# Kernel optimization log

Measured on AMD Instinct MI355X. Metric: run time of the kernel, lower is better.

## Reference

```python
import jax, jax.numpy as jnp
import numpy as np

B, N, DIM, H, DH, M = 2, 2048, 1024, 16, 64, 512
INNER = H * DH  # 1024
KV = M + 1 + N  # xl mem + null kv + sequence = 2561


def rotate_half(x):
    x1, x2 = jnp.split(x, 2, axis=-1)
    return jnp.concatenate([-x2, x1], axis=-1)


def apply_rotary_pos_emb(pos, t):
    return t * jnp.cos(pos) + rotate_half(t) * jnp.sin(pos)


def setup_inputs() -> dict:
    key = jax.random.key(0)
    ks = jax.random.split(key, 8)
    return {
        "x": jax.random.normal(ks[0], (B, N, DIM), jnp.float32),
        "rotary_q": jax.random.uniform(ks[1], (N, DH), jnp.float32) * 6.28,
        "rotary_k": jax.random.uniform(ks[2], (KV, DH), jnp.float32) * 6.28,
        "xl_memories": jax.random.normal(ks[3], (2, B, H, M, DH), jnp.float32) * 0.02,
        "Wq": jax.random.normal(ks[4], (DIM, INNER), jnp.float32) * 0.02,
        "Wkv": jax.random.normal(ks[5], (DIM, 2 * INNER), jnp.float32) * 0.02,
        "Wout": jax.random.normal(ks[6], (INNER, INNER), jnp.float32) * 0.02,
        "null_kv": jax.random.normal(ks[7], (2, H, DH), jnp.float32),
    }


def reference(x, rotary_q, rotary_k, xl_memories, Wq, Wkv, Wout, null_kv):
    # QKV projections (no bias, matching keras Dense(use_bias=False))
    q = (x @ Wq).reshape(B, N, H, DH).transpose(0, 2, 1, 3)  # b h n d
    k, v = jnp.split(x @ Wkv, 2, axis=-1)
    k = k.reshape(B, N, H, DH).transpose(0, 2, 1, 3)
    v = v.reshape(B, N, H, DH).transpose(0, 2, 1, 3)

    # prepend learned null key/value (1 token)
    nk = jnp.broadcast_to(null_kv[0][None, :, None, :], (B, H, 1, DH))
    nv = jnp.broadcast_to(null_kv[1][None, :, None, :], (B, H, 1, DH))
    k = jnp.concatenate([nk, k], axis=2)
    v = jnp.concatenate([nv, v], axis=2)

    next_xl_memories = jnp.stack([k, v])  # [2, b, h, 1+n, d]

    # prepend XL memories along key axis
    k = jnp.concatenate([xl_memories[0], k], axis=2)  # b h kv d
    v = jnp.concatenate([xl_memories[1], v], axis=2)

    # inline rotary embedding on q and (full) k
    q = apply_rotary_pos_emb(rotary_q, q)
    k = apply_rotary_pos_emb(rotary_k, k)

    # causal attention with bottom-right aligned mask (mem/null tokens visible)
    scale = DH ** -0.5
    sim = jnp.einsum('bhid,bhjd->bhij', q, k) * scale  # b h n kv
    i = jnp.arange(N)[:, None]
    j = jnp.arange(KV)[None, :]
    causal_ok = j <= (i + (KV - N))
    sim = jnp.where(causal_ok, sim, jnp.finfo(sim.dtype).min)
    attn = jax.nn.softmax(sim, axis=-1)
    out = jnp.einsum('bhij,bhjd->bhid', attn, v)  # b h n d

    out = out.transpose(0, 2, 1, 3).reshape(B, N, INNER)
    return out @ Wout, next_xl_memories
```

## Files before the change

kernel.cpp:

```cpp
#include <hip/hip_runtime.h>
#include <hip/hip_bf16.h>


typedef short v8s __attribute__((ext_vector_type(8)));
typedef float v4f __attribute__((ext_vector_type(4)));

__device__ __forceinline__ float bf2f(unsigned short x) {
  return __uint_as_float(((unsigned)x) << 16);
}
__device__ __forceinline__ unsigned short f2bf(float f) {
  unsigned u = __float_as_uint(f);
  u += 0x7FFFu + ((u >> 16) & 1u);
  return (unsigned short)(u >> 16);
}

#if __has_builtin(__builtin_amdgcn_exp2f)
#define EXP2(x) __builtin_amdgcn_exp2f(x)
#else
#define EXP2(x) exp2f(x)
#endif

__device__ __forceinline__ void gld_lds16(const void* g, void* l) {
  __builtin_amdgcn_global_load_lds(
      (const __attribute__((address_space(1))) unsigned int*)g,
      (__attribute__((address_space(3))) unsigned int*)l, 16, 0, 0);
}

__device__ __forceinline__ unsigned pk_bf16(float lo, float hi) {
  union { __hip_bfloat162 h; unsigned u; } cv;
  cv.h = __float22bfloat162_rn(make_float2(lo, hi));
  return cv.u;
}

__global__ __launch_bounds__(256) void cvt_bf16(
    const float* __restrict__ S, unsigned short* __restrict__ D, int n4)
{
  const int i = blockIdx.x * 256 + threadIdx.x;
  if (i < n4) {
    const float4 v = ((const float4*)S)[i];
    ushort4 o;
    o.x = f2bf(v.x); o.y = f2bf(v.y); o.z = f2bf(v.z); o.w = f2bf(v.w);
    ((ushort4*)D)[i] = o;
  }
}

template <typename CT>
__global__ __launch_bounds__(256, 2) void gemm_bf16(
    const unsigned short* __restrict__ A,
    const unsigned short* __restrict__ WT,
    CT* __restrict__ C,
    int K, int ldc)
{
  __shared__ unsigned short As[128 * 64];
  __shared__ unsigned short Bs[128 * 64];
  const int tid  = threadIdx.x;
  const int wave = tid >> 6, lane = tid & 63;
  const int l15  = lane & 15, quad = lane >> 4;
  const int wm   = wave >> 1, wn = wave & 1;
  const int row0 = blockIdx.x * 128, col0 = blockIdx.y * 128;
  const int lrow = lane >> 3;
  const int gsw  = (lane & 7) ^ lrow;

  v4f acc[4][4];
  const v4f vzero = {0.f, 0.f, 0.f, 0.f};
#pragma unroll
  for (int i = 0; i < 4; ++i)
#pragma unroll
    for (int j = 0; j < 4; ++j) acc[i][j] = vzero;

  for (int k0 = 0; k0 < K; k0 += 64) {
    __syncthreads();
#pragma unroll
    for (int ro = 0; ro < 4; ++ro) {
      const int chunk = wave * 4 + ro;
      const int arow  = chunk * 8 + lrow;
      gld_lds16(A  + (size_t)(row0 + arow) * K + k0 + gsw * 8, As + chunk * 512);
      gld_lds16(WT + (size_t)(col0 + arow) * K + k0 + gsw * 8, Bs + chunk * 512);
    }
    __syncthreads();

    v8s af[4][2], bf[4][2];
#pragma unroll
    for (int tm = 0; tm < 4; ++tm) {
      const int r = wm * 64 + tm * 16 + l15;
#pragma unroll
      for (int kk = 0; kk < 2; ++kk) {
        const int slot = (kk * 4 + quad) ^ (r & 7);
        af[tm][kk] = *(const v8s*)(As + r * 64 + slot * 8);
      }
    }
#pragma unroll
    for (int tn = 0; tn < 4; ++tn) {
      const int r = wn * 64 + tn * 16 + l15;
#pragma unroll
      for (int kk = 0; kk < 2; ++kk) {
        const int slot = (kk * 4 + quad) ^ (r & 7);
        bf[tn][kk] = *(const v8s*)(Bs + r * 64 + slot * 8);
      }
    }
#pragma unroll
    for (int kk = 0; kk < 2; ++kk)
#pragma unroll
      for (int tm = 0; tm < 4; ++tm)
#pragma unroll
        for (int tn = 0; tn < 4; ++tn)
          acc[tm][tn] = __builtin_amdgcn_mfma_f32_16x16x32_bf16(
              af[tm][kk], bf[tn][kk], acc[tm][tn], 0, 0, 0);
  }

#pragma unroll
  for (int tm = 0; tm < 4; ++tm)
#pragma unroll
    for (int tn = 0; tn < 4; ++tn)
#pragma unroll
      for (int r = 0; r < 4; ++r) {
        const int row = row0 + wm * 64 + tm * 16 + quad * 4 + r;
        const int col = col0 + wn * 64 + tn * 16 + l15;
        if constexpr (sizeof(CT) == 2)
          C[(size_t)row * ldc + col] = (CT)f2bf(acc[tm][tn][r]);
        else
          C[(size_t)row * ldc + col] = (CT)acc[tm][tn][r];
      }
}

__global__ __launch_bounds__(256) void transpose_wt(
    const float* __restrict__ S0,
    const float* __restrict__ S1,
    int c0, int c1, int K,
    unsigned short* __restrict__ D)
{
  __shared__ float T[64][65];
  const int k0 = blockIdx.x * 64, n0 = blockIdx.y * 64;
  const int tid = threadIdx.x;
#pragma unroll
  for (int ro = 0; ro < 4; ++ro) {
    const int idx = ro * 256 + tid;
    const int kr = idx >> 4, ch = idx & 15;
    const int n = n0 + ch * 4;
    float4 val;
    if (n < c0) val = *(const float4*)(S0 + (size_t)(k0 + kr) * c0 + n);
    else        val = *(const float4*)(S1 + (size_t)(k0 + kr) * c1 + (n - c0));
    T[kr][ch * 4 + 0] = val.x; T[kr][ch * 4 + 1] = val.y;
    T[kr][ch * 4 + 2] = val.z; T[kr][ch * 4 + 3] = val.w;
  }
  __syncthreads();
#pragma unroll
  for (int ro = 0; ro < 2; ++ro) {
    const int idx = ro * 256 + tid;
    const int nl = idx >> 3, ch = idx & 7;
    __align__(16) unsigned short tmp[8];
#pragma unroll
    for (int e = 0; e < 8; ++e) tmp[e] = f2bf(T[ch * 8 + e][nl]);
    *(uint4*)(D + (size_t)(n0 + nl) * K + k0 + ch * 8) = *(const uint4*)tmp;
  }
}

__global__ __launch_bounds__(256) void assemble(
    const unsigned short* __restrict__ QKV,
    const float* __restrict__ rq,
    const float* __restrict__ rk,
    const float* __restrict__ xlm,
    const float* __restrict__ nkv,
    unsigned short* __restrict__ Qrot,
    unsigned short* __restrict__ Kf,
    unsigned short* __restrict__ Vn,
    float* __restrict__ nxl)
{
  const int gw = blockIdx.x * 4 + (threadIdx.x >> 6);
  const int d  = threadIdx.x & 63;
  const int RK = 32 * 2561;
  const int RQ = 32 * 2048;
  if (gw < RK) {
    const int bh = gw / 2561;
    const int j  = gw - bh * 2561;
    const int b  = bh >> 4, h = bh & 15;
    float kx, vx;
    if (j < 512) {
      const size_t i0 = (((size_t)(b * 16 + h)) * 512 + j) * 64 + d;
      kx = xlm[i0];
      vx = xlm[1048576 + i0];
    } else if (j == 512) {
      kx = nkv[h * 64 + d];
      vx = nkv[1024 + h * 64 + d];
    } else {
      const size_t rowb = ((size_t)(b * 2048 + (j - 513))) * 3072;
      kx = bf2f(QKV[rowb + 1024 + h * 64 + d]);
      vx = bf2f(QKV[rowb + 2048 + h * 64 + d]);
    }
    Vn[(((size_t)bh) * 2561 + j) * 64 + d] = f2bf(vx);
    if (j >= 512) {
      const size_t o0 = (((size_t)(b * 16 + h)) * 2049 + (j - 512)) * 64 + d;
      nxl[o0] = kx;
      nxl[4196352 + o0] = vx;
    }
    const float ang = rk[j * 64 + d];
    const float cs = __cosf(ang), sn = __sinf(ang);
    const float part = __shfl_xor(kx, 32);
    const float kr = kx * cs + (d < 32 ? -part : part) * sn;
    Kf[(((size_t)bh) * 2624 + j) * 64 + d] = f2bf(kr);
  } else if (gw < RK + RQ) {
    const int g2 = gw - RK;
    const int bh = g2 >> 11, n = g2 & 2047;
    const int b  = bh >> 4, h = bh & 15;
    const float qx = bf2f(QKV[((size_t)(b * 2048 + n)) * 3072 + h * 64 + d]);
    const float ang = rq[n * 64 + d];
    const float cs = __cosf(ang), sn = __sinf(ang);
    const float part = __shfl_xor(qx, 32);
    const float qr = qx * cs + (d < 32 ? -part : part) * sn;
    Qrot[(((size_t)bh) * 2048 + n) * 64 + d] = f2bf(qr * 0.18033688f);
  } else {
    const int g3 = gw - RK - RQ;
    const int bh = g3 / 63;
    const int jj = 2561 + (g3 - bh * 63);
    Kf[(((size_t)bh) * 2624 + jj) * 64 + d] = 0;
  }
}

__global__ __launch_bounds__(256) void transpose_v(
    const unsigned short* __restrict__ Vn,
    unsigned short* __restrict__ VTp)
{
  __shared__ unsigned short T[64][72];
  const int j0 = blockIdx.x * 64;
  const int bh = blockIdx.y;
  const int tid = threadIdx.x;
#pragma unroll
  for (int ro = 0; ro < 2; ++ro) {
    const int idx = ro * 256 + tid;
    const int jr = idx >> 3, ch = idx & 7;
    uint4 val = make_uint4(0, 0, 0, 0);
    if (j0 + jr < 2561)
      val = *(const uint4*)(Vn + (((size_t)bh) * 2561 + j0 + jr) * 64 + ch * 8);
    *(uint4*)(&T[jr][ch * 8]) = val;
  }
  __syncthreads();
#pragma unroll
  for (int ro = 0; ro < 2; ++ro) {
    const int idx = ro * 256 + tid;
    const int dl = idx >> 3, ch = idx & 7;
    __align__(16) unsigned short tmp[8];
#pragma unroll
    for (int e = 0; e < 8; ++e) {
      const int kappa = ch * 8 + e;
      const int sig = (kappa & 32) + ((e & 4) << 2) + ((ch & 3) << 2) + (e & 3);
      tmp[e] = T[sig][dl];
    }
    *(uint4*)(VTp + (((size_t)bh) * 64 + dl) * 2624 + j0 + ch * 8) = *(const uint4*)tmp;
  }
}

__global__ __launch_bounds__(128, 2) void attn_fa(
    const unsigned short* __restrict__ Qr,
    const unsigned short* __restrict__ Kf,
    const unsigned short* __restrict__ VTp,
    unsigned short* __restrict__ Ao)
{
  const int bh = blockIdx.y;
  const int qb = 31 - (int)((blockIdx.x + blockIdx.y) & 31);
  const int b = bh >> 4, h = bh & 15;
  __shared__ unsigned short Ks[2][64 * 72];
  __shared__ unsigned short Vs[2][64 * 72];
  const int tid = threadIdx.x;
  const int wave = tid >> 6;
  const int lane = tid & 63;
  const int l15 = lane & 15, quad = lane >> 4;
  const v4f vzero = {0.f, 0.f, 0.f, 0.f};

  v8s qf00, qf01, qf10, qf11;
  {
    const unsigned short* Qg0 =
        Qr + (((size_t)bh) * 2048 + qb * 64 + wave * 32 + l15) * 64;
    qf00 = *(const v8s*)(Qg0 + quad * 8);
    qf01 = *(const v8s*)(Qg0 + 32 + quad * 8);
    const unsigned short* Qg1 = Qg0 + 16 * 64;
    qf10 = *(const v8s*)(Qg1 + quad * 8);
    qf11 = *(const v8s*)(Qg1 + 32 + quad * 8);
  }
  const int qb0 = qb * 64 + wave * 32 + l15 + 513;

  v4f O00 = vzero, O01 = vzero, O02 = vzero, O03 = vzero;
  v4f O10 = vzero, O11 = vzero, O12 = vzero, O13 = vzero;
  v4f Ol0 = vzero, Ol1 = vzero;
  const short one_bf = (short)0x3F80;
  const v8s ones = {one_bf, one_bf, one_bf, one_bf,
                    one_bf, one_bf, one_bf, one_bf};

  const unsigned short* Kg0 = Kf + (size_t)bh * 2624 * 64;
  const unsigned short* Vg0 = VTp + (size_t)bh * 64 * 2624;
  const int ntiles = (qb + 10 <= 41) ? (qb + 10) : 41;
  const int tfast  = qb + 7;

  const int srow = tid >> 3, sch = tid & 7;
  uint4 kk0, kk1, kk2, kk3, vv0, vv1, vv2, vv3;

#define PREFETCH(t)                                                          \
  {                                                                          \
    const int j0p = (t) * 64;                                                \
    kk0 = *(const uint4*)(Kg0 + (size_t)(j0p + srow)      * 64 + sch * 8);   \
    kk1 = *(const uint4*)(Kg0 + (size_t)(j0p + srow + 16) * 64 + sch * 8);   \
    kk2 = *(const uint4*)(Kg0 + (size_t)(j0p + srow + 32) * 64 + sch * 8);   \
    kk3 = *(const uint4*)(Kg0 + (size_t)(j0p + srow + 48) * 64 + sch * 8);   \
    vv0 = *(const uint4*)(Vg0 + (size_t)(srow)      * 2624 + j0p + sch * 8); \
    vv1 = *(const uint4*)(Vg0 + (size_t)(srow + 16) * 2624 + j0p + sch * 8); \
    vv2 = *(const uint4*)(Vg0 + (size_t)(srow + 32) * 2624 + j0p + sch * 8); \
    vv3 = *(const uint4*)(Vg0 + (size_t)(srow + 48) * 2624 + j0p + sch * 8); \
  }
#define STAGE(bi)                                                            \
  {                                                                          \
    *(uint4*)(Ks[bi] + (srow)      * 72 + sch * 8) = kk0;                    \
    *(uint4*)(Ks[bi] + (srow + 16) * 72 + sch * 8) = kk1;                    \
    *(uint4*)(Ks[bi] + (srow + 32) * 72 + sch * 8) = kk2;                    \
    *(uint4*)(Ks[bi] + (srow + 48) * 72 + sch * 8) = kk3;                    \
    *(uint4*)(Vs[bi] + (srow)      * 72 + sch * 8) = vv0;                    \
    *(uint4*)(Vs[bi] + (srow + 16) * 72 + sch * 8) = vv1;                    \
    *(uint4*)(Vs[bi] + (srow + 32) * 72 + sch * 8) = vv2;                    \
    *(uint4*)(Vs[bi] + (srow + 48) * 72 + sch * 8) = vv3;                    \
  }

  auto compute_tile = [&](const unsigned short* Ksb, const unsigned short* Vsb,
                          int j0, bool masked) {
    v4f s[2][4];
#pragma unroll
    for (int jt = 0; jt < 4; ++jt) {
      const v8s kfr0 = *(const v8s*)(Ksb + (jt * 16 + l15) * 72 + quad * 8);
      const v8s kfr1 = *(const v8s*)(Ksb + (jt * 16 + l15) * 72 + 32 + quad * 8);
      v4f c0 = vzero;
      c0 = __builtin_amdgcn_mfma_f32_16x16x32_bf16(kfr0, qf00, c0, 0, 0, 0);
      c0 = __builtin_amdgcn_mfma_f32_16x16x32_bf16(kfr1, qf01, c0, 0, 0, 0);
      s[0][jt] = c0;
      v4f c1 = vzero;
      c1 = __builtin_amdgcn_mfma_f32_16x16x32_bf16(kfr0, qf10, c1, 0, 0, 0);
      c1 = __builtin_amdgcn_mfma_f32_16x16x32_bf16(kfr1, qf11, c1, 0, 0, 0);
      s[1][jt] = c1;
    }

    if (masked) {
#pragma unroll
      for (int mt = 0; mt < 2; ++mt) {
        const int qbase = qb0 + mt * 16;
#pragma unroll
        for (int jt = 0; jt < 4; ++jt) {
          const int jrow = j0 + jt * 16 + quad * 4;
#pragma unroll
          for (int r = 0; r < 4; ++r)
            s[mt][jt][r] = (jrow + r <= qbase) ? s[mt][jt][r] : -1e30f;
        }
      }
    }

    union PK { unsigned u[4]; v8s s8; };
    PK p0a, p0b, p1a, p1b;
    p0a.u[0] = pk_bf16(EXP2(s[0][0][0]), EXP2(s[0][0][1]));
    p0a.u[1] = pk_bf16(EXP2(s[0][0][2]), EXP2(s[0][0][3]));
    p0a.u[2] = pk_bf16(EXP2(s[0][1][0]), EXP2(s[0][1][1]));
    p0a.u[3] = pk_bf16(EXP2(s[0][1][2]), EXP2(s[0][1][3]));
    p0b.u[0] = pk_bf16(EXP2(s[0][2][0]), EXP2(s[0][2][1]));
    p0b.u[1] = pk_bf16(EXP2(s[0][2][2]), EXP2(s[0][2][3]));
    p0b.u[2] = pk_bf16(EXP2(s[0][3][0]), EXP2(s[0][3][1]));
    p0b.u[3] = pk_bf16(EXP2(s[0][3][2]), EXP2(s[0][3][3]));
    p1a.u[0] = pk_bf16(EXP2(s[1][0][0]), EXP2(s[1][0][1]));
    p1a.u[1] = pk_bf16(EXP2(s[1][0][2]), EXP2(s[1][0][3]));
    p1a.u[2] = pk_bf16(EXP2(s[1][1][0]), EXP2(s[1][1][1]));
    p1a.u[3] = pk_bf16(EXP2(s[1][1][2]), EXP2(s[1][1][3]));
    p1b.u[0] = pk_bf16(EXP2(s[1][2][0]), EXP2(s[1][2][1]));
    p1b.u[1] = pk_bf16(EXP2(s[1][2][2]), EXP2(s[1][2][3]));
    p1b.u[2] = pk_bf16(EXP2(s[1][3][0]), EXP2(s[1][3][1]));
    p1b.u[3] = pk_bf16(EXP2(s[1][3][2]), EXP2(s[1][3][3]));

#pragma unroll
    for (int dt = 0; dt < 4; ++dt) {
      const v8s vf0 = *(const v8s*)(Vsb + (dt * 16 + l15) * 72 + quad * 8);
      const v8s vf1 = *(const v8s*)(Vsb + (dt * 16 + l15) * 72 + 32 + quad * 8);
      v4f c0 = (dt == 0) ? O00 : (dt == 1) ? O01 : (dt == 2) ? O02 : O03;
      c0 = __builtin_amdgcn_mfma_f32_16x16x32_bf16(p0a.s8, vf0, c0, 0, 0, 0);
      c0 = __builtin_amdgcn_mfma_f32_16x16x32_bf16(p0b.s8, vf1, c0, 0, 0, 0);
      if (dt == 0) O00 = c0; else if (dt == 1) O01 = c0;
      else if (dt == 2) O02 = c0; else O03 = c0;
      v4f c1 = (dt == 0) ? O10 : (dt == 1) ? O11 : (dt == 2) ? O12 : O13;
      c1 = __builtin_amdgcn_mfma_f32_16x16x32_bf16(p1a.s8, vf0, c1, 0, 0, 0);
      c1 = __builtin_amdgcn_mfma_f32_16x16x32_bf16(p1b.s8, vf1, c1, 0, 0, 0);
      if (dt == 0) O10 = c1; else if (dt == 1) O11 = c1;
      else if (dt == 2) O12 = c1; else O13 = c1;
    }
    Ol0 = __builtin_amdgcn_mfma_f32_16x16x32_bf16(p0a.s8, ones, Ol0, 0, 0, 0);
    Ol0 = __builtin_amdgcn_mfma_f32_16x16x32_bf16(p0b.s8, ones, Ol0, 0, 0, 0);
    Ol1 = __builtin_amdgcn_mfma_f32_16x16x32_bf16(p1a.s8, ones, Ol1, 0, 0, 0);
    Ol1 = __builtin_amdgcn_mfma_f32_16x16x32_bf16(p1b.s8, ones, Ol1, 0, 0, 0);
  };

  PREFETCH(0);
  STAGE(0);
  PREFETCH(1);
  __syncthreads();
  for (int t = 0; t < ntiles; ++t) {
    if (t + 1 < ntiles) {
      STAGE((t + 1) & 1);
      if (t + 2 < ntiles) PREFETCH(t + 2);
    }
    compute_tile(Ks[t & 1], Vs[t & 1], t * 64, t > tfast);
    __syncthreads();
  }
#undef PREFETCH
#undef STAGE

#pragma unroll
  for (int r = 0; r < 4; ++r) {
    const float linv0 = 1.0f / Ol0[r];
    const int n0 = qb * 64 + wave * 32 + quad * 4 + r;
    const size_t rb0 = ((size_t)b * 2048 + n0) * 1024 + h * 64;
    Ao[rb0 + 0 * 16 + l15] = f2bf(O00[r] * linv0);
    Ao[rb0 + 1 * 16 + l15] = f2bf(O01[r] * linv0);
    Ao[rb0 + 2 * 16 + l15] = f2bf(O02[r] * linv0);
    Ao[rb0 + 3 * 16 + l15] = f2bf(O03[r] * linv0);
    const float linv1 = 1.0f / Ol1[r];
    const size_t rb1 = rb0 + (size_t)16 * 1024;
    Ao[rb1 + 0 * 16 + l15] = f2bf(O10[r] * linv1);
    Ao[rb1 + 1 * 16 + l15] = f2bf(O11[r] * linv1);
    Ao[rb1 + 2 * 16 + l15] = f2bf(O12[r] * linv1);
    Ao[rb1 + 3 * 16 + l15] = f2bf(O13[r] * linv1);
  }
}

extern "C" void kernel_launch(void* const* d_in, const int* in_sizes, int n_in,
                              void* d_out, int out_size, void* d_ws, size_t ws_size,
                              hipStream_t stream)
{
  const float* x    = (const float*)d_in[0];
  const float* rq   = (const float*)d_in[1];
  const float* rk   = (const float*)d_in[2];
  const float* xlm  = (const float*)d_in[3];
  const float* Wq   = (const float*)d_in[4];
  const float* Wkv  = (const float*)d_in[5];
  const float* Wout = (const float*)d_in[6];
  const float* nkv  = (const float*)d_in[7];
  float* out = (float*)d_out;
  float* nxl = out + 4194304;
  char* ws = (char*)d_ws;
  unsigned short* QKV   = (unsigned short*)(ws + 0);
  unsigned short* xbf   = (unsigned short*)(ws + 25165824);
  unsigned short* Ao    = (unsigned short*)(ws + 25165824);
  unsigned short* WqkvT = (unsigned short*)(ws + 33554432);
  unsigned short* WoutT = (unsigned short*)(ws + 39845888);
  unsigned short* Qrot  = (unsigned short*)(ws + 41943040);
  unsigned short* Kf    = (unsigned short*)(ws + 50331648);
  unsigned short* Vn    = (unsigned short*)(ws + 61079552);
  unsigned short* VTp   = (unsigned short*)(ws + 71569408);

  cvt_bf16<<<4096, 256, 0, stream>>>(x, xbf, 1048576);
  transpose_wt<<<dim3(16, 48), 256, 0, stream>>>(Wq, Wkv, 1024, 2048, 1024, WqkvT);
  transpose_wt<<<dim3(16, 16), 256, 0, stream>>>(Wout, Wout, 1024, 1024, 1024, WoutT);
  gemm_bf16<unsigned short><<<dim3(32, 24), 256, 0, stream>>>(xbf, WqkvT, QKV, 1024, 3072);
  assemble<<<37376, 256, 0, stream>>>(QKV, rq, rk, xlm, nkv, Qrot, Kf, Vn, nxl);
  transpose_v<<<dim3(41, 32), 256, 0, stream>>>(Vn, VTp);
  attn_fa<<<dim3(32, 32), 128, 0, stream>>>(Qrot, Kf, VTp, Ao);
  gemm_bf16<float><<<dim3(32, 8), 256, 0, stream>>>(Ao, WoutT, out, 1024, 1024);
}
```

Before: 241.8 us.

## Split KV range across two wave pairs in attention with LDS reduction

The attention block grows from 2 to 4 waves. Two wave pairs each process half of the KV tiles using 32-wide KV tiles, and their partial O and row-sum accumulators are combined through shared memory at the end. This doubles parallelism per query block to hide latency on the long causal KV loop. In exchange it adds a final LDS reduction and an extra barrier, uses smaller tiles with more loop iterations, and puts more register and occupancy pressure on the kernel under launch_bounds(256,4).

```diff
diff --git a/kernel.cpp b/kernel.cpp
--- a/kernel.cpp
+++ b/kernel.cpp
@@ -249,7 +249,7 @@
   }
 }
 
-__global__ __launch_bounds__(128, 2) void attn_fa(
+__global__ __launch_bounds__(256, 4) void attn_fa(
     const unsigned short* __restrict__ Qr,
     const unsigned short* __restrict__ Kf,
     const unsigned short* __restrict__ VTp,
@@ -258,10 +258,12 @@
   const int bh = blockIdx.y;
   const int qb = 31 - (int)((blockIdx.x + blockIdx.y) & 31);
   const int b = bh >> 4, h = bh & 15;
-  __shared__ unsigned short Ks[2][64 * 72];
-  __shared__ unsigned short Vs[2][64 * 72];
+  __shared__ unsigned short Ks[2][2][32 * 72];
+  __shared__ unsigned short Vs[2][2][64 * 40];
   const int tid = threadIdx.x;
   const int wave = tid >> 6;
+  const int wr  = wave & 1;
+  const int kvh = wave >> 1;
   const int lane = tid & 63;
   const int l15 = lane & 15, quad = lane >> 4;
   const v4f vzero = {0.f, 0.f, 0.f, 0.f};
@@ -269,14 +271,14 @@
   v8s qf00, qf01, qf10, qf11;
   {
     const unsigned short* Qg0 =
-        Qr + (((size_t)bh) * 2048 + qb * 64 + wave * 32 + l15) * 64;
+        Qr + (((size_t)bh) * 2048 + qb * 64 + wr * 32 + l15) * 64;
     qf00 = *(const v8s*)(Qg0 + quad * 8);
     qf01 = *(const v8s*)(Qg0 + 32 + quad * 8);
     const unsigned short* Qg1 = Qg0 + 16 * 64;
     qf10 = *(const v8s*)(Qg1 + quad * 8);
     qf11 = *(const v8s*)(Qg1 + 32 + quad * 8);
   }
-  const int qb0 = qb * 64 + wave * 32 + l15 + 513;
+  const int qb0 = qb * 64 + wr * 32 + l15 + 513;
 
   v4f O00 = vzero, O01 = vzero, O02 = vzero, O03 = vzero;
   v4f O10 = vzero, O11 = vzero, O12 = vzero, O13 = vzero;
@@ -287,137 +289,148 @@
 
   const unsigned short* Kg0 = Kf + (size_t)bh * 2624 * 64;
   const unsigned short* Vg0 = VTp + (size_t)bh * 64 * 2624;
-  const int ntiles = (qb + 10 <= 41) ? (qb + 10) : 41;
-  const int tfast  = qb + 7;
-
-  const int srow = tid >> 3, sch = tid & 7;
-  uint4 kk0, kk1, kk2, kk3, vv0, vv1, vv2, vv3;
+  const int nt32  = (2 * qb + 19 <= 81) ? (2 * qb + 19) : 81;
+  const int nh    = (nt32 + 1) >> 1;
+  const int tbase = kvh ? nh : 0;
+  const int tcnt  = kvh ? (nt32 - nh) : nh;
+  const int tfast = 2 * qb + wr + 15;
+
+  const int ptid = tid & 127;
+  const int krow = ptid >> 3, ksch = ptid & 7;
+  const int vrow = ptid >> 2, vscv = ptid & 3;
+  uint4 kk0, kk1, vv0, vv1;
 
 #define PREFETCH(t)                                                          \
   {                                                                          \
-    const int j0p = (t) * 64;                                                \
-    kk0 = *(const uint4*)(Kg0 + (size_t)(j0p + srow)      * 64 + sch * 8);   \
-    kk1 = *(const uint4*)(Kg0 + (size_t)(j0p + srow + 16) * 64 + sch * 8);   \
-    kk2 = *(const uint4*)(Kg0 + (size_t)(j0p + srow + 32) * 64 + sch * 8);   \
-    kk3 = *(const uint4*)(Kg0 + (size_t)(j0p + srow + 48) * 64 + sch * 8);   \
-    vv0 = *(const uint4*)(Vg0 + (size_t)(srow)      * 2624 + j0p + sch * 8); \
-    vv1 = *(const uint4*)(Vg0 + (size_t)(srow + 16) * 2624 + j0p + sch * 8); \
-    vv2 = *(const uint4*)(Vg0 + (size_t)(srow + 32) * 2624 + j0p + sch * 8); \
-    vv3 = *(const uint4*)(Vg0 + (size_t)(srow + 48) * 2624 + j0p + sch * 8); \
+    const int j0p = (t) * 32;                                                \
+    kk0 = *(const uint4*)(Kg0 + (size_t)(j0p + krow)      * 64 + ksch * 8);  \
+    kk1 = *(const uint4*)(Kg0 + (size_t)(j0p + krow + 16) * 64 + ksch * 8);  \
+    vv0 = *(const uint4*)(Vg0 + (size_t)(vrow)      * 2624 + j0p + vscv * 8);\
+    vv1 = *(const uint4*)(Vg0 + (size_t)(vrow + 32) * 2624 + j0p + vscv * 8);\
   }
 #define STAGE(bi)                                                            \
   {                                                                          \
-    *(uint4*)(Ks[bi] + (srow)      * 72 + sch * 8) = kk0;                    \
-    *(uint4*)(Ks[bi] + (srow + 16) * 72 + sch * 8) = kk1;                    \
-    *(uint4*)(Ks[bi] + (srow + 32) * 72 + sch * 8) = kk2;                    \
-    *(uint4*)(Ks[bi] + (srow + 48) * 72 + sch * 8) = kk3;                    \
-    *(uint4*)(Vs[bi] + (srow)      * 72 + sch * 8) = vv0;                    \
-    *(uint4*)(Vs[bi] + (srow + 16) * 72 + sch * 8) = vv1;                    \
-    *(uint4*)(Vs[bi] + (srow + 32) * 72 + sch * 8) = vv2;                    \
-    *(uint4*)(Vs[bi] + (srow + 48) * 72 + sch * 8) = vv3;                    \
+    *(uint4*)(Ks[kvh][bi] + (krow)      * 72 + ksch * 8) = kk0;              \
+    *(uint4*)(Ks[kvh][bi] + (krow + 16) * 72 + ksch * 8) = kk1;              \
+    *(uint4*)(Vs[kvh][bi] + (vrow)      * 40 + vscv * 8) = vv0;              \
+    *(uint4*)(Vs[kvh][bi] + (vrow + 32) * 40 + vscv * 8) = vv1;              \
   }
 
   auto compute_tile = [&](const unsigned short* Ksb, const unsigned short* Vsb,
-                          int j0, bool masked) {
-    v4f s[2][4];
-#pragma unroll
-    for (int jt = 0; jt < 4; ++jt) {
-      const v8s kfr0 = *(const v8s*)(Ksb + (jt * 16 + l15) * 72 + quad * 8);
-      const v8s kfr1 = *(const v8s*)(Ksb + (jt * 16 + l15) * 72 + 32 + quad * 8);
-      v4f c0 = vzero;
-      c0 = __builtin_amdgcn_mfma_f32_16x16x32_bf16(kfr0, qf00, c0, 0, 0, 0);
-      c0 = __builtin_amdgcn_mfma_f32_16x16x32_bf16(kfr1, qf01, c0, 0, 0, 0);
-      s[0][jt] = c0;
-      v4f c1 = vzero;
-      c1 = __builtin_amdgcn_mfma_f32_16x16x32_bf16(kfr0, qf10, c1, 0, 0, 0);
-      c1 = __builtin_amdgcn_mfma_f32_16x16x32_bf16(kfr1, qf11, c1, 0, 0, 0);
-      s[1][jt] = c1;
-    }
-
-    if (masked) {
-#pragma unroll
-      for (int mt = 0; mt < 2; ++mt) {
-        const int qbase = qb0 + mt * 16;
-#pragma unroll
-        for (int jt = 0; jt < 4; ++jt) {
-          const int jrow = j0 + jt * 16 + quad * 4;
-#pragma unroll
-          for (int r = 0; r < 4; ++r)
-            s[mt][jt][r] = (jrow + r <= qbase) ? s[mt][jt][r] : -1e30f;
-        }
+                          int t) {
+    v4f s00, s01, s10, s11;
+    {
+      const v8s ka0 = *(const v8s*)(Ksb + l15 * 72 + quad * 8);
+      const v8s ka1 = *(const v8s*)(Ksb + l15 * 72 + 32 + quad * 8);
+      v4f c = vzero;
+      c = __builtin_amdgcn_mfma_f32_16x16x32_bf16(ka0, qf00, c, 0, 0, 0);
+      c = __builtin_amdgcn_mfma_f32_16x16x32_bf16(ka1, qf01, c, 0, 0, 0);
+      s00 = c;
+      c = vzero;
+      c = __builtin_amdgcn_mfma_f32_16x16x32_bf16(ka0, qf10, c, 0, 0, 0);
+      c = __builtin_amdgcn_mfma_f32_16x16x32_bf16(ka1, qf11, c, 0, 0, 0);
+      s10 = c;
+      const v8s kb0 = *(const v8s*)(Ksb + (16 + l15) * 72 + quad * 8);
+      const v8s kb1 = *(const v8s*)(Ksb + (16 + l15) * 72 + 32 + quad * 8);
+      c = vzero;
+      c = __builtin_amdgcn_mfma_f32_16x16x32_bf16(kb0, qf00, c, 0, 0, 0);
+      c = __builtin_amdgcn_mfma_f32_16x16x32_bf16(kb1, qf01, c, 0, 0, 0);
+      s01 = c;
+      c = vzero;
+      c = __builtin_amdgcn_mfma_f32_16x16x32_bf16(kb0, qf10, c, 0, 0, 0);
+      c = __builtin_amdgcn_mfma_f32_16x16x32_bf16(kb1, qf11, c, 0, 0, 0);
+      s11 = c;
+    }
+
+    if (t > tfast) {
+      const int j0 = t * 32 + quad * 4;
+#pragma unroll
+      for (int r = 0; r < 4; ++r) {
+        s00[r] = (j0 + r      <= qb0)      ? s00[r] : -1e30f;
+        s01[r] = (j0 + 16 + r <= qb0)      ? s01[r] : -1e30f;
+        s10[r] = (j0 + r      <= qb0 + 16) ? s10[r] : -1e30f;
+        s11[r] = (j0 + 16 + r <= qb0 + 16) ? s11[r] : -1e30f;
       }
     }
 
     union PK { unsigned u[4]; v8s s8; };
-    PK p0a, p0b, p1a, p1b;
-    p0a.u[0] = pk_bf16(EXP2(s[0][0][0]), EXP2(s[0][0][1]));
-    p0a.u[1] = pk_bf16(EXP2(s[0][0][2]), EXP2(s[0][0][3]));
-    p0a.u[2] = pk_bf16(EXP2(s[0][1][0]), EXP2(s[0][1][1]));
-    p0a.u[3] = pk_bf16(EXP2(s[0][1][2]), EXP2(s[0][1][3]));
-    p0b.u[0] = pk_bf16(EXP2(s[0][2][0]), EXP2(s[0][2][1]));
-    p0b.u[1] = pk_bf16(EXP2(s[0][2][2]), EXP2(s[0][2][3]));
-    p0b.u[2] = pk_bf16(EXP2(s[0][3][0]), EXP2(s[0][3][1]));
-    p0b.u[3] = pk_bf16(EXP2(s[0][3][2]), EXP2(s[0][3][3]));
-    p1a.u[0] = pk_bf16(EXP2(s[1][0][0]), EXP2(s[1][0][1]));
-    p1a.u[1] = pk_bf16(EXP2(s[1][0][2]), EXP2(s[1][0][3]));
-    p1a.u[2] = pk_bf16(EXP2(s[1][1][0]), EXP2(s[1][1][1]));
-    p1a.u[3] = pk_bf16(EXP2(s[1][1][2]), EXP2(s[1][1][3]));
-    p1b.u[0] = pk_bf16(EXP2(s[1][2][0]), EXP2(s[1][2][1]));
-    p1b.u[1] = pk_bf16(EXP2(s[1][2][2]), EXP2(s[1][2][3]));
-    p1b.u[2] = pk_bf16(EXP2(s[1][3][0]), EXP2(s[1][3][1]));
-    p1b.u[3] = pk_bf16(EXP2(s[1][3][2]), EXP2(s[1][3][3]));
-
-#pragma unroll
-    for (int dt = 0; dt < 4; ++dt) {
-      const v8s vf0 = *(const v8s*)(Vsb + (dt * 16 + l15) * 72 + quad * 8);
-      const v8s vf1 = *(const v8s*)(Vsb + (dt * 16 + l15) * 72 + 32 + quad * 8);
-      v4f c0 = (dt == 0) ? O00 : (dt == 1) ? O01 : (dt == 2) ? O02 : O03;
-      c0 = __builtin_amdgcn_mfma_f32_16x16x32_bf16(p0a.s8, vf0, c0, 0, 0, 0);
-      c0 = __builtin_amdgcn_mfma_f32_16x16x32_bf16(p0b.s8, vf1, c0, 0, 0, 0);
-      if (dt == 0) O00 = c0; else if (dt == 1) O01 = c0;
-      else if (dt == 2) O02 = c0; else O03 = c0;
-      v4f c1 = (dt == 0) ? O10 : (dt == 1) ? O11 : (dt == 2) ? O12 : O13;
-      c1 = __builtin_amdgcn_mfma_f32_16x16x32_bf16(p1a.s8, vf0, c1, 0, 0, 0);
-      c1 = __builtin_amdgcn_mfma_f32_16x16x32_bf16(p1b.s8, vf1, c1, 0, 0, 0);
-      if (dt == 0) O10 = c1; else if (dt == 1) O11 = c1;
-      else if (dt == 2) O12 = c1; else O13 = c1;
-    }
-    Ol0 = __builtin_amdgcn_mfma_f32_16x16x32_bf16(p0a.s8, ones, Ol0, 0, 0, 0);
-    Ol0 = __builtin_amdgcn_mfma_f32_16x16x32_bf16(p0b.s8, ones, Ol0, 0, 0, 0);
-    Ol1 = __builtin_amdgcn_mfma_f32_16x16x32_bf16(p1a.s8, ones, Ol1, 0, 0, 0);
-    Ol1 = __builtin_amdgcn_mfma_f32_16x16x32_bf16(p1b.s8, ones, Ol1, 0, 0, 0);
+    PK p0, p1;
+    p0.u[0] = pk_bf16(EXP2(s00[0]), EXP2(s00[1]));
+    p0.u[1] = pk_bf16(EXP2(s00[2]), EXP2(s00[3]));
+    p0.u[2] = pk_bf16(EXP2(s01[0]), EXP2(s01[1]));
+    p0.u[3] = pk_bf16(EXP2(s01[2]), EXP2(s01[3]));
+    p1.u[0] = pk_bf16(EXP2(s10[0]), EXP2(s10[1]));
+    p1.u[1] = pk_bf16(EXP2(s10[2]), EXP2(s10[3]));
+    p1.u[2] = pk_bf16(EXP2(s11[0]), EXP2(s11[1]));
+    p1.u[3] = pk_bf16(EXP2(s11[2]), EXP2(s11[3]));
+
+    {
+      const v8s vf0 = *(const v8s*)(Vsb + l15 * 40 + quad * 8);
+      O00 = __builtin_amdgcn_mfma_f32_16x16x32_bf16(p0.s8, vf0, O00, 0, 0, 0);
+      O10 = __builtin_amdgcn_mfma_f32_16x16x32_bf16(p1.s8, vf0, O10, 0, 0, 0);
+      const v8s vf1 = *(const v8s*)(Vsb + (16 + l15) * 40 + quad * 8);
+      O01 = __builtin_amdgcn_mfma_f32_16x16x32_bf16(p0.s8, vf1, O01, 0, 0, 0);
+      O11 = __builtin_amdgcn_mfma_f32_16x16x32_bf16(p1.s8, vf1, O11, 0, 0, 0);
+      const v8s vf2 = *(const v8s*)(Vsb + (32 + l15) * 40 + quad * 8);
+      O02 = __builtin_amdgcn_mfma_f32_16x16x32_bf16(p0.s8, vf2, O02, 0, 0, 0);
+      O12 = __builtin_amdgcn_mfma_f32_16x16x32_bf16(p1.s8, vf2, O12, 0, 0, 0);
+      const v8s vf3 = *(const v8s*)(Vsb + (48 + l15) * 40 + quad * 8);
+      O03 = __builtin_amdgcn_mfma_f32_16x16x32_bf16(p0.s8, vf3, O03, 0, 0, 0);
+      O13 = __builtin_amdgcn_mfma_f32_16x16x32_bf16(p1.s8, vf3, O13, 0, 0, 0);
+    }
+    Ol0 = __builtin_amdgcn_mfma_f32_16x16x32_bf16(p0.s8, ones, Ol0, 0, 0, 0);
+    Ol1 = __builtin_amdgcn_mfma_f32_16x16x32_bf16(p1.s8, ones, Ol1, 0, 0, 0);
   };
 
-  PREFETCH(0);
+  PREFETCH(tbase);
   STAGE(0);
-  PREFETCH(1);
+  PREFETCH(tbase + 1);
   __syncthreads();
-  for (int t = 0; t < ntiles; ++t) {
-    if (t + 1 < ntiles) {
-      STAGE((t + 1) & 1);
-      if (t + 2 < ntiles) PREFETCH(t + 2);
-    }
-    compute_tile(Ks[t & 1], Vs[t & 1], t * 64, t > tfast);
+  for (int it = 0; it < nh; ++it) {
+    if (it < tcnt) {
+      if (it + 1 < tcnt) {
+        STAGE((it + 1) & 1);
+        if (it + 2 < tcnt) PREFETCH(tbase + it + 2);
+      }
+      compute_tile(Ks[kvh][it & 1], Vs[kvh][it & 1], tbase + it);
+    }
     __syncthreads();
   }
 #undef PREFETCH
 #undef STAGE
 
-#pragma unroll
-  for (int r = 0; r < 4; ++r) {
-    const float linv0 = 1.0f / Ol0[r];
-    const int n0 = qb * 64 + wave * 32 + quad * 4 + r;
-    const size_t rb0 = ((size_t)b * 2048 + n0) * 1024 + h * 64;
-    Ao[rb0 + 0 * 16 + l15] = f2bf(O00[r] * linv0);
-    Ao[rb0 + 1 * 16 + l15] = f2bf(O01[r] * linv0);
-    Ao[rb0 + 2 * 16 + l15] = f2bf(O02[r] * linv0);
-    Ao[rb0 + 3 * 16 + l15] = f2bf(O03[r] * linv0);
-    const float linv1 = 1.0f / Ol1[r];
-    const size_t rb1 = rb0 + (size_t)16 * 1024;
-    Ao[rb1 + 0 * 16 + l15] = f2bf(O10[r] * linv1);
-    Ao[rb1 + 1 * 16 + l15] = f2bf(O11[r] * linv1);
-    Ao[rb1 + 2 * 16 + l15] = f2bf(O12[r] * linv1);
-    Ao[rb1 + 3 * 16 + l15] = f2bf(O13[r] * linv1);
+  float* R = (float*)(&Vs[0][0][0]);
+  float* Rb = R + ((size_t)wr * 64 + lane) * 40;
+  if (kvh == 1) {
+    *(v4f*)(Rb + 0)  = O00; *(v4f*)(Rb + 4)  = O01;
+    *(v4f*)(Rb + 8)  = O02; *(v4f*)(Rb + 12) = O03;
+    *(v4f*)(Rb + 16) = O10; *(v4f*)(Rb + 20) = O11;
+    *(v4f*)(Rb + 24) = O12; *(v4f*)(Rb + 28) = O13;
+    *(v4f*)(Rb + 32) = Ol0; *(v4f*)(Rb + 36) = Ol1;
+  }
+  __syncthreads();
+  if (kvh == 0) {
+    O00 += *(const v4f*)(Rb + 0);  O01 += *(const v4f*)(Rb + 4);
+    O02 += *(const v4f*)(Rb + 8);  O03 += *(const v4f*)(Rb + 12);
+    O10 += *(const v4f*)(Rb + 16); O11 += *(const v4f*)(Rb + 20);
+    O12 += *(const v4f*)(Rb + 24); O13 += *(const v4f*)(Rb + 28);
+    Ol0 += *(const v4f*)(Rb + 32); Ol1 += *(const v4f*)(Rb + 36);
+#pragma unroll
+    for (int r = 0; r < 4; ++r) {
+      const float linv0 = 1.0f / Ol0[r];
+      const int n0 = qb * 64 + wr * 32 + quad * 4 + r;
+      const size_t rb0 = ((size_t)b * 2048 + n0) * 1024 + h * 64;
+      Ao[rb0 + 0 * 16 + l15] = f2bf(O00[r] * linv0);
+      Ao[rb0 + 1 * 16 + l15] = f2bf(O01[r] * linv0);
+      Ao[rb0 + 2 * 16 + l15] = f2bf(O02[r] * linv0);
+      Ao[rb0 + 3 * 16 + l15] = f2bf(O03[r] * linv0);
+      const float linv1 = 1.0f / Ol1[r];
+      const size_t rb1 = rb0 + (size_t)16 * 1024;
+      Ao[rb1 + 0 * 16 + l15] = f2bf(O10[r] * linv1);
+      Ao[rb1 + 1 * 16 + l15] = f2bf(O11[r] * linv1);
+      Ao[rb1 + 2 * 16 + l15] = f2bf(O12[r] * linv1);
+      Ao[rb1 + 3 * 16 + l15] = f2bf(O13[r] * linv1);
+    }
   }
 }
 
@@ -452,6 +465,6 @@
   gemm_bf16<unsigned short><<<dim3(32, 24), 256, 0, stream>>>(xbf, WqkvT, QKV, 1024, 3072);
   assemble<<<37376, 256, 0, stream>>>(QKV, rq, rk, xlm, nkv, Qrot, Kf, Vn, nxl);
   transpose_v<<<dim3(41, 32), 256, 0, stream>>>(Vn, VTp);
-  attn_fa<<<dim3(32, 32), 128, 0, stream>>>(Qrot, Kf, VTp, Ao);
+  attn_fa<<<dim3(32, 32), 256, 0, stream>>>(Qrot, Kf, VTp, Ao);
   gemm_bf16<float><<<dim3(32, 8), 256, 0, stream>>>(Ao, WoutT, out, 1024, 1024);
 }
```

New measurement: 243.0 us. About the same (+0.5%).
